# Kernel optimization log

Hardware: AMD Instinct MI355X
Metric: run time of the kernel (lower is better)

The kernel has to match this reference:

```python
import jax, jax.numpy as jnp
import numpy as np

NOISE_EPS = 1e-2   # Shazeer noisy-gating stddev floor
LN_EPS = 1e-6
LOSS_COEF = 0.01
K = 2              # num_activated_experts


def _layer_norm(x, w, b):
    mu = jnp.mean(x, axis=-1, keepdims=True)
    var = jnp.var(x, axis=-1, keepdims=True)
    return (x - mu) * jax.lax.rsqrt(var + LN_EPS) * w + b


def _cv_squared(v):
    return jnp.var(v) / (jnp.mean(v) ** 2 + 1e-10)


def _normal_cdf(z):
    return 0.5 * (1.0 + jax.scipy.special.erf(z / jnp.sqrt(jnp.asarray(2.0, z.dtype))))


def setup_inputs() -> dict:
    key = jax.random.key(0)
    ks = jax.random.split(key, 8)
    N, D, H, O, E = 8192, 512, 1024, 512, 8
    x = jax.random.normal(ks[0], (N, D), jnp.float32)
    x_offsets = jnp.sort(jax.random.randint(ks[1], (17,), 0, N)).astype(jnp.int64)
    noise = jax.random.normal(ks[2], (N, E), jnp.float32)
    s = 0.02
    return {
        "x": x,
        "x_offsets": x_offsets,
        "max_seq_len": 2048,
        "noise": noise,
        "norm_w": jnp.ones((D,), jnp.float32),
        "norm_bias": jnp.zeros((D,), jnp.float32),
        "w_gate": jax.random.normal(ks[3], (D, E), jnp.float32) * s,
        "w_noise": jax.random.normal(ks[4], (D, E), jnp.float32) * s,
        "W1": jax.random.normal(ks[5], (E, H, D), jnp.float32) * s,  # [E, model_d, input]
        "b1": jnp.zeros((E, H), jnp.float32),
        "W2": jax.random.normal(ks[6], (E, O, H), jnp.float32) * s,  # [E, output, model_d]
        "b2": jnp.zeros((E, O), jnp.float32),
        "output_weight": jax.random.normal(ks[7], (D, O), jnp.float32) * s,
    }


def reference(x, x_offsets, max_seq_len, noise, norm_w, norm_bias, w_gate, w_noise,
              W1, b1, W2, b2, output_weight):
    N, D = x.shape
    E = w_gate.shape[1]
    k_plus = min(K + 1, E)

    # pre-norm
    x_norm = _layer_norm(x, norm_w, norm_bias)

    # noisy top-k gating (training path)
    clean_logits = x_norm @ w_gate                      # [N, E]
    noise_stddev = jax.nn.softplus(x_norm @ w_noise) + NOISE_EPS
    noisy_logits = clean_logits + noise * noise_stddev

    top_logits, top_indices = jax.lax.top_k(noisy_logits, k_plus)   # [N, k+1]
    top_k_logits = top_logits[:, :K]
    top_k_indices = top_indices[:, :K]
    top_k_gates = jax.nn.softmax(top_k_logits, axis=-1)             # [N, K]

    rows = jnp.arange(N)[:, None]
    gates = jnp.zeros((N, E), top_k_gates.dtype).at[rows, top_k_indices].set(top_k_gates)

    # load = prob each expert is in top-k under the gating noise (Shazeer)
    flat = top_logits.reshape(-1)
    pos_in = jnp.arange(N) * k_plus + K
    thr_in = flat[pos_in][:, None]          # (k+1)-th value: threshold if already in
    thr_out = flat[pos_in - 1][:, None]     # k-th value: threshold if currently out
    is_in = noisy_logits > thr_in
    prob_in = _normal_cdf((clean_logits - thr_in) / noise_stddev)
    prob_out = _normal_cdf((clean_logits - thr_out) / noise_stddev)
    load_probs = jnp.where(is_in, prob_in, prob_out)                # [N, E]

    loss = LOSS_COEF * (_cv_squared(gates.sum(0)) + _cv_squared(load_probs.sum(0)))

    # dispatch stats: tokens per expert
    lengths = jnp.zeros((E,), jnp.float32).at[top_k_indices.reshape(-1)].add(1.0)
    load = lengths / lengths.sum()

    # grouped expert MLP (dense one-hot combine; gates are 0 for unrouted experts)
    h = jnp.einsum('nd,ehd->neh', x_norm, W1) + b1                  # [N, E, H]
    a = jax.nn.silu(h)
    y_e = jnp.einsum('neh,eoh->neo', a, W2) + b2                    # [N, E, O]
    y_moe = jnp.einsum('ne,neo->no', gates, y_e)                    # [N, O]

    # shared expert: addmm(y, shared_x=x, output_weight)
    y = y_moe + x @ output_weight
    return y, loss, load
```

## Files before the change

kernel.cpp:

```cpp
#include <hip/hip_runtime.h>
#include <math.h>

typedef unsigned short u16;
typedef unsigned int u32;

#define N_ROWS 8192
#define DDIM 512
#define HDIM 1024
#define ODIM 512
#define NEXP 8
#define MAXPAIRS (N_ROWS * 2)
#define MAXPOS (MAXPAIRS + NEXP * 128)
#define MAXTILES (MAXPOS / 128)

#define SM_CNT 0
#define SM_CUR 8
#define SM_AOFF 16
#define SM_GSUM 32
#define SM_LSUM 40
#define SM_WORDS 64

using short8 = __attribute__((ext_vector_type(8))) short;
using float4v = __attribute__((ext_vector_type(4))) float;

__device__ __forceinline__ u16 f2bf(float f) {
    union { float f; u32 u; } v; v.f = f;
    u32 u = v.u;
    return (u16)((u + 0x7fffu + ((u >> 16) & 1u)) >> 16);
}

__device__ __forceinline__ void async_copy16(u16* lds, const u16* g) {
    __builtin_amdgcn_global_load_lds(
        (const __attribute__((address_space(1))) void*)g,
        (__attribute__((address_space(3))) void*)lds, 16, 0, 0);
}

__global__ __launch_bounds__(512) void init1_kernel(int* small, float* zeropage) {
    int i = threadIdx.x;
    if (i < SM_WORDS) small[i] = 0;
    zeropage[i] = 0.f;
}

#define W1CONV_BLOCKS 4096
#define GATE_BLOCKS 512
#define OWT_BLOCKS 256
#define BUCKET_BLOCKS 68
#define YZERO_BLOCKS 1024
__global__ __launch_bounds__(256) void combo_kernel(
    const float* __restrict__ x, const float* __restrict__ noise,
    const float* __restrict__ norm_w, const float* __restrict__ norm_b,
    const float* __restrict__ w_gate, const float* __restrict__ w_noise,
    const float* __restrict__ W1, const float* __restrict__ ow,
    u16* __restrict__ xnorm_bf, u16* __restrict__ x_bf,
    int* __restrict__ pair_expert, float* __restrict__ pair_gate,
    u16* __restrict__ W1b, u16* __restrict__ owT,
    int* __restrict__ small, int* __restrict__ bucket_rows, float* __restrict__ y)
{
    __shared__ __align__(16) float sh[NEXP * DDIM * 2 + 64];
    int b = blockIdx.x, tid = threadIdx.x;

    if (b >= GATE_BLOCKS) {
        int cb = b - GATE_BLOCKS;
        if (cb < W1CONV_BLOCKS) {
            size_t i = (size_t)cb * 256 + tid;
            float4 v = ((const float4*)W1)[i];
            ushort4 o;
            o.x = f2bf(v.x); o.y = f2bf(v.y); o.z = f2bf(v.z); o.w = f2bf(v.w);
            ((ushort4*)W1b)[i] = o;
        } else if (cb < W1CONV_BLOCKS + OWT_BLOCKS) {
            float (*tile)[33] = (float(*)[33])sh;
            int t = cb - W1CONV_BLOCKS;
            int bx = (t & 15) * 32, by = (t >> 4) * 32;
            int tx = tid & 31, ty = tid >> 5;
            for (int r = ty; r < 32; r += 8) tile[r][tx] = ow[(size_t)(by + r) * ODIM + bx + tx];
            __syncthreads();
            for (int r = ty; r < 32; r += 8) owT[(size_t)(bx + r) * DDIM + by + tx] = f2bf(tile[tx][r]);
        } else if (cb < W1CONV_BLOCKS + OWT_BLOCKS + BUCKET_BLOCKS) {
            int i = (cb - W1CONV_BLOCKS - OWT_BLOCKS) * 256 + tid;
            if (i < MAXPOS) bucket_rows[i] = -1;
        } else {
            int zb = cb - W1CONV_BLOCKS - OWT_BLOCKS - BUCKET_BLOCKS;
            size_t i = (size_t)zb * 1024 + tid;
            float4 zero = {0.f, 0.f, 0.f, 0.f};
#pragma unroll
            for (int t = 0; t < 4; t++, i += 256) ((float4*)y)[i] = zero;
        }
        return;
    }

    float* wgT = sh;
    float* wnT = sh + NEXP * DDIM;
    float* blk_g = sh + 2 * NEXP * DDIM;
    float* blk_l = blk_g + NEXP;
    int* blk_c = (int*)(blk_l + NEXP);
    float* smf = (float*)small;

    for (int i = tid; i < NEXP * DDIM; i += 256) {
        int d = i >> 3, e = i & 7;
        wgT[e * DDIM + d] = w_gate[i];
        wnT[e * DDIM + d] = w_noise[i];
    }
    if (tid < NEXP) { blk_g[tid] = 0.f; blk_l[tid] = 0.f; blk_c[tid] = 0; }
    __syncthreads();

    int wave = tid >> 6, lane = tid & 63;
    float nw[8], nb[8];
#pragma unroll
    for (int j = 0; j < 8; j++) { nw[j] = norm_w[j * 64 + lane]; nb[j] = norm_b[j * 64 + lane]; }

    for (int r = 0; r < 4; ++r) {
        int row = b * 16 + wave * 4 + r;
        const float* xr = x + (size_t)row * DDIM;
        float xv[8], s = 0.f, s2 = 0.f;
#pragma unroll
        for (int j = 0; j < 8; j++) { float v = xr[j * 64 + lane]; xv[j] = v; s += v; s2 += v * v; }
#pragma unroll
        for (int o = 32; o; o >>= 1) { s += __shfl_xor(s, o, 64); s2 += __shfl_xor(s2, o, 64); }
        float mu = s * (1.f / DDIM);
        float var = s2 * (1.f / DDIM) - mu * mu;
        float rstd = rsqrtf(var + 1e-6f);

        float acc[16];
#pragma unroll
        for (int e = 0; e < 16; e++) acc[e] = 0.f;
#pragma unroll
        for (int j = 0; j < 8; j++) {
            float v = (xv[j] - mu) * rstd * nw[j] + nb[j];
            int d = j * 64 + lane;
            xnorm_bf[(size_t)row * DDIM + d] = f2bf(v);
            x_bf[(size_t)row * DDIM + d] = f2bf(xv[j]);
#pragma unroll
            for (int e = 0; e < 8; e++) {
                acc[e] += v * wgT[e * DDIM + d];
                acc[8 + e] += v * wnT[e * DDIM + d];
            }
        }
#pragma unroll
        for (int e = 0; e < 16; e++)
#pragma unroll
            for (int o = 32; o; o >>= 1) acc[e] += __shfl_xor(acc[e], o, 64);

        float cl[8], sd[8], nz[8];
#pragma unroll
        for (int e = 0; e < 8; e++) {
            cl[e] = acc[e];
            float t = acc[8 + e];
            float sp = fmaxf(t, 0.f) + log1pf(expf(-fabsf(t)));
            sd[e] = sp + 0.01f;
            nz[e] = cl[e] + noise[(size_t)row * NEXP + e] * sd[e];
        }
        int idx[3]; float val[3]; u32 msk = 0;
#pragma unroll
        for (int t = 0; t < 3; t++) {
            float best = -INFINITY; int bi = 0;
#pragma unroll
            for (int e = 0; e < 8; e++)
                if (!((msk >> e) & 1) && nz[e] > best) { best = nz[e]; bi = e; }
            idx[t] = bi; val[t] = best; msk |= 1u << bi;
        }
        float e1 = expf(val[1] - val[0]);
        float g0 = 1.f / (1.f + e1), g1 = e1 / (1.f + e1);
        float thr_in = val[2], thr_out = val[1];

        if (lane == 0) {
            pair_expert[row * 2] = idx[0]; pair_gate[row * 2] = g0;
            pair_expert[row * 2 + 1] = idx[1]; pair_gate[row * 2 + 1] = g1;
            atomicAdd(&blk_g[idx[0]], g0); atomicAdd(&blk_g[idx[1]], g1);
            atomicAdd(&blk_c[idx[0]], 1); atomicAdd(&blk_c[idx[1]], 1);
#pragma unroll
            for (int e = 0; e < 8; e++) {
                float thr = (nz[e] > thr_in) ? thr_in : thr_out;
                float z = (cl[e] - thr) / sd[e];
                float p = 0.5f * (1.f + erff(z * 0.70710678118654752f));
                atomicAdd(&blk_l[e], p);
            }
        }
    }
    __syncthreads();
    if (tid < NEXP) {
        atomicAdd(smf + SM_GSUM + tid, blk_g[tid]);
        atomicAdd(smf + SM_LSUM + tid, blk_l[tid]);
        atomicAdd(&small[SM_CNT + tid], blk_c[tid]);
    }
}

__global__ __launch_bounds__(256) void scatter_kernel(
    const int* __restrict__ pair_expert, const float* __restrict__ pair_gate,
    int* __restrict__ small, int* __restrict__ bucket_rows, float* __restrict__ gate_by_pos,
    float* __restrict__ out_loss, float* __restrict__ out_load)
{
    __shared__ int aoff[NEXP + 1];
    __shared__ int blk_cnt[NEXP];
    __shared__ int blk_base[NEXP];
    int tid = threadIdx.x;
    if (tid == 0) {
        int acc = 0; aoff[0] = 0;
        for (int e = 0; e < NEXP; e++) { acc += (small[SM_CNT + e] + 127) & ~127; aoff[e + 1] = acc; }
    }
    if (tid < NEXP) blk_cnt[tid] = 0;
    __syncthreads();
    int p = blockIdx.x * 256 + tid;
    int e = pair_expert[p];
    int local = atomicAdd(&blk_cnt[e], 1);
    __syncthreads();
    if (tid < NEXP)
        blk_base[tid] = aoff[tid] + atomicAdd(&small[SM_CUR + tid], blk_cnt[tid]);
    if (blockIdx.x == 0 && tid < NEXP + 1) small[SM_AOFF + tid] = aoff[tid];
    __syncthreads();
    int pos = blk_base[e] + local;
    bucket_rows[pos] = p >> 1;
    gate_by_pos[pos] = pair_gate[p];

    if (blockIdx.x == 0 && tid == 0) {
        const float* gs = (const float*)small + SM_GSUM;
        const float* ls = (const float*)small + SM_LSUM;
        float cv[2];
        for (int t = 0; t < 2; t++) {
            const float* v = t ? ls : gs;
            float m = 0.f;
            for (int k = 0; k < NEXP; k++) m += v[k];
            m *= (1.f / NEXP);
            float var = 0.f;
            for (int k = 0; k < NEXP; k++) { float d = v[k] - m; var += d * d; }
            var *= (1.f / NEXP);
            cv[t] = var / (m * m + 1e-10f);
        }
        out_loss[0] = 0.01f * (cv[0] + cv[1]);
        int tot = 0;
        for (int k = 0; k < NEXP; k++) tot += small[SM_CNT + k];
        float inv = 1.f / (float)tot;
        for (int k = 0; k < NEXP; k++) out_load[k] = (float)small[SM_CNT + k] * inv;
    }
}

__global__ __launch_bounds__(256) void gemmA_kernel(
    const u16* __restrict__ xnorm, const u16* __restrict__ W1b,
    const float* __restrict__ W2, u16* __restrict__ W2b,
    const int* __restrict__ bucket_rows, const int* __restrict__ small,
    const float* __restrict__ b1, const u16* __restrict__ zeropage,
    u16* __restrict__ a_buf)
{
    constexpr int KD = 512;
    __shared__ __align__(16) u16 As[128 * 64];
    __shared__ __align__(16) u16 Bs[128 * 64];

    int tid = threadIdx.x;
    if (blockIdx.y >= 8) {
        int j = (blockIdx.y - 8) * 136 + blockIdx.x;
        if (j >= 2048) return;
        size_t i = (size_t)j * 512 + tid;
#pragma unroll
        for (int t = 0; t < 2; t++, i += 256) {
            float4 v = ((const float4*)W2)[i];
            ushort4 o;
            o.x = f2bf(v.x); o.y = f2bf(v.y); o.z = f2bf(v.z); o.w = f2bf(v.w);
            ((ushort4*)W2b)[i] = o;
        }
        return;
    }

    int base = blockIdx.x * 128;
    if (base >= small[SM_AOFF + 8]) return;
    int e = 0;
    while (e < 7 && base >= small[SM_AOFF + e + 1]) ++e;
    int bn = blockIdx.y * 128;
    const u16* Bsel = W1b + (size_t)e * HDIM * KD;

    int wave = tid >> 6, lane = tid & 63;
    int lr = lane >> 3;
    int lc = ((lane & 7) ^ lr) * 8;

    const u16* ga[4]; const u16* gb[4];
    u16* la[4]; u16* lb[4];
#pragma unroll
    for (int c = 0; c < 4; c++) {
        int tr = wave * 32 + c * 8;
        int r0 = bucket_rows[base + tr + lr];
        ga[c] = ((r0 < 0) ? zeropage : xnorm + (size_t)r0 * KD) + lc;
        gb[c] = Bsel + (size_t)(bn + tr + lr) * KD + lc;
        la[c] = &As[tr * 64];
        lb[c] = &Bs[tr * 64];
    }

    int wm = (wave & 1) * 64, wn = (wave >> 1) * 64;
    int fr = lane & 15, kq = lane >> 4, f7 = fr & 7;

    float4v acc[4][4];
#pragma unroll
    for (int i = 0; i < 4; i++)
#pragma unroll
        for (int j = 0; j < 4; j++) acc[i][j] = (float4v){0.f, 0.f, 0.f, 0.f};

    for (int k0 = 0; k0 < KD; k0 += 64) {
        __syncthreads();
#pragma unroll
        for (int c = 0; c < 4; c++) async_copy16(la[c], ga[c] + k0);
#pragma unroll
        for (int c = 0; c < 4; c++) async_copy16(lb[c], gb[c] + k0);
        __syncthreads();
        short8 af[4][2], bf[4][2];
#pragma unroll
        for (int mt = 0; mt < 4; mt++)
#pragma unroll
            for (int kh = 0; kh < 2; kh++)
                af[mt][kh] = *(const short8*)&As[(wm + mt * 16 + fr) * 64 + (((kq + 4 * kh) ^ f7) * 8)];
#pragma unroll
        for (int nt = 0; nt < 4; nt++)
#pragma unroll
            for (int kh = 0; kh < 2; kh++)
                bf[nt][kh] = *(const short8*)&Bs[(wn + nt * 16 + fr) * 64 + (((kq + 4 * kh) ^ f7) * 8)];
#pragma unroll
        for (int mt = 0; mt < 4; mt++)
#pragma unroll
            for (int nt = 0; nt < 4; nt++) {
                acc[mt][nt] = __builtin_amdgcn_mfma_f32_16x16x32_bf16(af[mt][0], bf[nt][0], acc[mt][nt], 0, 0, 0);
                acc[mt][nt] = __builtin_amdgcn_mfma_f32_16x16x32_bf16(af[mt][1], bf[nt][1], acc[mt][nt], 0, 0, 0);
            }
    }

    int rbase = (lane >> 4) * 4, c16 = lane & 15;
#pragma unroll
    for (int nt = 0; nt < 4; nt++) {
        int gn = bn + wn + nt * 16 + c16;
        float bv = b1[e * HDIM + gn];
#pragma unroll
        for (int mt = 0; mt < 4; mt++) {
            int gm = base + wm + mt * 16 + rbase;
#pragma unroll
            for (int r = 0; r < 4; r++) {
                float h = acc[mt][nt][r] + bv;
                float a = h * __builtin_amdgcn_rcpf(1.f + __expf(-h));
                a_buf[(size_t)(gm + r) * HDIM + gn] = f2bf(a);
            }
        }
    }
}

__global__ __launch_bounds__(256) void gemmB_kernel(
    const u16* __restrict__ a_buf, const u16* __restrict__ W2b,
    const u16* __restrict__ xbf, const u16* __restrict__ owT,
    const int* __restrict__ bucket_rows, const int* __restrict__ small,
    const float* __restrict__ b2, const float* __restrict__ gate_by_pos,
    float* __restrict__ y)
{
    __shared__ __align__(16) u16 As[2][128 * 32];
    __shared__ __align__(16) u16 Bs[2][128 * 32];

    int tid = threadIdx.x;
    int wave = tid >> 6, lane = tid & 63;
    const int lrow = lane >> 2;
    const int kcol = (((lane & 3) ^ ((lane >> 3) & 3)) * 8);
    const int trow = wave * 32 + lrow;
    int wm = (wave & 1) * 64, wn = (wave >> 1) * 64;
    int fr = lane & 15, kq = lane >> 4;
    const int kg = ((kq ^ ((fr >> 1) & 3)) * 8);

    bool expertPath = blockIdx.y < 4;
    int base, bn, e = 0, KD;
    const u16 *ga0, *ga1, *gb0, *gb1;
    if (expertPath) {
        KD = 1024;
        base = blockIdx.x * 128;
        if (base >= small[SM_AOFF + 8]) return;
        while (e < 7 && base >= small[SM_AOFF + e + 1]) ++e;
        bn = blockIdx.y * 128;
        ga0 = a_buf + (size_t)(base + trow) * KD + kcol;
        ga1 = a_buf + (size_t)(base + trow + 16) * KD + kcol;
        const u16* Bsel = W2b + (size_t)e * ODIM * KD;
        gb0 = Bsel + (size_t)(bn + trow) * KD + kcol;
        gb1 = Bsel + (size_t)(bn + trow + 16) * KD + kcol;
    } else {
        KD = 512;
        int j = (blockIdx.y - 4) * 136 + blockIdx.x;
        if (j >= 256) return;
        base = (j >> 2) * 128;
        bn = (j & 3) * 128;
        ga0 = xbf + (size_t)(base + trow) * KD + kcol;
        ga1 = xbf + (size_t)(base + trow + 16) * KD + kcol;
        gb0 = owT + (size_t)(bn + trow) * KD + kcol;
        gb1 = owT + (size_t)(bn + trow + 16) * KD + kcol;
    }
    const int ofA0 = (wave * 32) * 32;
    const int ofA1 = (wave * 32 + 16) * 32;

    float4v acc[4][4];
#pragma unroll
    for (int i = 0; i < 4; i++)
#pragma unroll
        for (int j = 0; j < 4; j++) acc[i][j] = (float4v){0.f, 0.f, 0.f, 0.f};

    const int nk = KD >> 5;
    async_copy16(&As[0][ofA0], ga0);
    async_copy16(&As[0][ofA1], ga1);
    async_copy16(&Bs[0][ofA0], gb0);
    async_copy16(&Bs[0][ofA1], gb1);
    __syncthreads();

    int cur = 0;
    for (int t = 0; t < nk; ++t) {
        int nxt = cur ^ 1;
        if (t + 1 < nk) {
            int k1 = (t + 1) << 5;
            async_copy16(&As[nxt][ofA0], ga0 + k1);
            async_copy16(&As[nxt][ofA1], ga1 + k1);
            async_copy16(&Bs[nxt][ofA0], gb0 + k1);
            async_copy16(&Bs[nxt][ofA1], gb1 + k1);
        }
        short8 af[4], bf[4];
#pragma unroll
        for (int mt = 0; mt < 4; mt++) af[mt] = *(const short8*)&As[cur][(wm + mt * 16 + fr) * 32 + kg];
#pragma unroll
        for (int nt = 0; nt < 4; nt++) bf[nt] = *(const short8*)&Bs[cur][(wn + nt * 16 + fr) * 32 + kg];
#pragma unroll
        for (int mt = 0; mt < 4; mt++)
#pragma unroll
            for (int nt = 0; nt < 4; nt++)
                acc[mt][nt] = __builtin_amdgcn_mfma_f32_16x16x32_bf16(af[mt], bf[nt], acc[mt][nt], 0, 0, 0);
        __syncthreads();
        cur = nxt;
    }

    int rbase = (lane >> 4) * 4, c16 = lane & 15;
    if (expertPath) {
#pragma unroll
        for (int mt = 0; mt < 4; mt++) {
            int pos0 = base + wm + mt * 16 + rbase;
            int rows[4]; float gs[4];
#pragma unroll
            for (int r = 0; r < 4; r++) { rows[r] = bucket_rows[pos0 + r]; gs[r] = gate_by_pos[pos0 + r]; }
#pragma unroll
            for (int nt = 0; nt < 4; nt++) {
                int gn = bn + wn + nt * 16 + c16;
                float b2v = b2[e * ODIM + gn];
#pragma unroll
                for (int r = 0; r < 4; r++) {
                    if (rows[r] >= 0)
                        unsafeAtomicAdd(&y[(size_t)rows[r] * ODIM + gn], gs[r] * (acc[mt][nt][r] + b2v));
                }
            }
        }
    } else {
#pragma unroll
        for (int mt = 0; mt < 4; mt++) {
            int gm = base + wm + mt * 16 + rbase;
#pragma unroll
            for (int nt = 0; nt < 4; nt++) {
                int gn = bn + wn + nt * 16 + c16;
#pragma unroll
                for (int r = 0; r < 4; r++)
                    unsafeAtomicAdd(&y[(size_t)(gm + r) * ODIM + gn], acc[mt][nt][r]);
            }
        }
    }
}

extern "C" void kernel_launch(void* const* d_in, const int* in_sizes, int n_in,
                              void* d_out, int out_size, void* d_ws, size_t ws_size,
                              hipStream_t stream)
{
    (void)in_sizes; (void)n_in; (void)out_size; (void)ws_size;
    const float* x = (const float*)d_in[0];
    const float* noise = (const float*)d_in[3];
    const float* norm_w = (const float*)d_in[4];
    const float* norm_b = (const float*)d_in[5];
    const float* w_gate = (const float*)d_in[6];
    const float* w_noise = (const float*)d_in[7];
    const float* W1 = (const float*)d_in[8];
    const float* b1 = (const float*)d_in[9];
    const float* W2 = (const float*)d_in[10];
    const float* b2 = (const float*)d_in[11];
    const float* ow = (const float*)d_in[12];

    float* y = (float*)d_out;
    float* out_loss = y + (size_t)N_ROWS * ODIM;
    float* out_load = out_loss + 1;

    char* ws = (char*)d_ws;
    size_t off = 0;
    auto alloc = [&](size_t b) { size_t p = off; off = (off + b + 255) & ~(size_t)255; return p; };
    u16* xnorm_bf = (u16*)(ws + alloc((size_t)N_ROWS * DDIM * 2));
    u16* x_bf     = (u16*)(ws + alloc((size_t)N_ROWS * DDIM * 2));
    u16* W1b      = (u16*)(ws + alloc((size_t)NEXP * HDIM * DDIM * 2));
    u16* W2b      = (u16*)(ws + alloc((size_t)NEXP * ODIM * HDIM * 2));
    u16* owT      = (u16*)(ws + alloc((size_t)DDIM * ODIM * 2));
    u16* a_buf    = (u16*)(ws + alloc((size_t)MAXPOS * HDIM * 2));
    int* pair_expert = (int*)(ws + alloc((size_t)MAXPAIRS * 4));
    float* pair_gate = (float*)(ws + alloc((size_t)MAXPAIRS * 4));
    float* gate_by_pos = (float*)(ws + alloc((size_t)MAXPOS * 4));
    int* bucket_rows = (int*)(ws + alloc((size_t)MAXPOS * 4));
    int* small       = (int*)(ws + alloc(SM_WORDS * 4));
    float* zeropage  = (float*)(ws + alloc(2048));

    init1_kernel<<<1, 512, 0, stream>>>(small, zeropage);
    combo_kernel<<<GATE_BLOCKS + W1CONV_BLOCKS + OWT_BLOCKS + BUCKET_BLOCKS + YZERO_BLOCKS,
                   256, 0, stream>>>(
        x, noise, norm_w, norm_b, w_gate, w_noise, W1, ow,
        xnorm_bf, x_bf, pair_expert, pair_gate, W1b, owT, small, bucket_rows, y);
    scatter_kernel<<<MAXPAIRS / 256, 256, 0, stream>>>(pair_expert, pair_gate, small,
                                                       bucket_rows, gate_by_pos, out_loss, out_load);
    gemmA_kernel<<<dim3(MAXTILES, 8 + 16), 256, 0, stream>>>(xnorm_bf, W1b, W2, W2b,
                                                             bucket_rows, small, b1,
                                                             (const u16*)zeropage, a_buf);
    gemmB_kernel<<<dim3(MAXTILES, 6), 256, 0, stream>>>(a_buf, W2b, x_bf, owT, bucket_rows,
                                                        small, b2, gate_by_pos, y);
}
```

Before: 247.1 us.

## Triple-buffer LDS tiles in both expert GEMMs with a single-barrier prefetch pipeline

Both grouped GEMM kernels move to a three-stage shared-memory ring of 32-wide K slices. Loads are issued two slices ahead, and each iteration waits with a partial vmcnt and a single barrier. The first GEMM was previously unpipelined, with two syncthreads and no overlap. The change also raises wave priority around the MFMA block with s_setprio. The goal is to hide global-to-LDS latency behind the matrix math, at the cost of more shared memory per block and reliance on hand-placed waitcnt counts being correct.

Result: slower. 281.5 us (+13.9%).

```diff
diff --git a/kernel.cpp b/kernel.cpp
--- a/kernel.cpp
+++ b/kernel.cpp
@@ -241,8 +241,8 @@
     u16* __restrict__ a_buf)
 {
     constexpr int KD = 512;
-    __shared__ __align__(16) u16 As[128 * 64];
-    __shared__ __align__(16) u16 Bs[128 * 64];
+    __shared__ __align__(16) u16 As[3][128 * 32];
+    __shared__ __align__(16) u16 Bs[3][128 * 32];
 
     int tid = threadIdx.x;
     if (blockIdx.y >= 8) {
@@ -267,23 +267,21 @@
     const u16* Bsel = W1b + (size_t)e * HDIM * KD;
 
     int wave = tid >> 6, lane = tid & 63;
-    int lr = lane >> 3;
-    int lc = ((lane & 7) ^ lr) * 8;
-
-    const u16* ga[4]; const u16* gb[4];
-    u16* la[4]; u16* lb[4];
-#pragma unroll
-    for (int c = 0; c < 4; c++) {
-        int tr = wave * 32 + c * 8;
-        int r0 = bucket_rows[base + tr + lr];
-        ga[c] = ((r0 < 0) ? zeropage : xnorm + (size_t)r0 * KD) + lc;
-        gb[c] = Bsel + (size_t)(bn + tr + lr) * KD + lc;
-        la[c] = &As[tr * 64];
-        lb[c] = &Bs[tr * 64];
-    }
-
+    const int lrow = lane >> 2;
+    const int kcol = (((lane & 3) ^ ((lane >> 3) & 3)) * 8);
+    const int trow = wave * 32 + lrow;
     int wm = (wave & 1) * 64, wn = (wave >> 1) * 64;
-    int fr = lane & 15, kq = lane >> 4, f7 = fr & 7;
+    int fr = lane & 15, kq = lane >> 4;
+    const int kg = ((kq ^ ((fr >> 1) & 3)) * 8);
+
+    int r0 = bucket_rows[base + trow];
+    int r1 = bucket_rows[base + trow + 16];
+    const u16* ga0 = ((r0 < 0) ? zeropage : xnorm + (size_t)r0 * KD) + kcol;
+    const u16* ga1 = ((r1 < 0) ? zeropage : xnorm + (size_t)r1 * KD) + kcol;
+    const u16* gb0 = Bsel + (size_t)(bn + trow) * KD + kcol;
+    const u16* gb1 = Bsel + (size_t)(bn + trow + 16) * KD + kcol;
+    const int ofA0 = (wave * 32) * 32;
+    const int ofA1 = (wave * 32 + 16) * 32;
 
     float4v acc[4][4];
 #pragma unroll
@@ -291,31 +289,37 @@
 #pragma unroll
         for (int j = 0; j < 4; j++) acc[i][j] = (float4v){0.f, 0.f, 0.f, 0.f};
 
-    for (int k0 = 0; k0 < KD; k0 += 64) {
-        __syncthreads();
-#pragma unroll
-        for (int c = 0; c < 4; c++) async_copy16(la[c], ga[c] + k0);
-#pragma unroll
-        for (int c = 0; c < 4; c++) async_copy16(lb[c], gb[c] + k0);
-        __syncthreads();
-        short8 af[4][2], bf[4][2];
+    constexpr int nk = KD >> 5;
+    async_copy16(&As[0][ofA0], ga0);      async_copy16(&As[0][ofA1], ga1);
+    async_copy16(&Bs[0][ofA0], gb0);      async_copy16(&Bs[0][ofA1], gb1);
+    async_copy16(&As[1][ofA0], ga0 + 32); async_copy16(&As[1][ofA1], ga1 + 32);
+    async_copy16(&Bs[1][ofA0], gb0 + 32); async_copy16(&Bs[1][ofA1], gb1 + 32);
+
+    int cur = 0;
+    for (int t = 0; t < nk; ++t) {
+        if (t == nk - 1) asm volatile("s_waitcnt vmcnt(0)" ::: "memory");
+        else             asm volatile("s_waitcnt vmcnt(4)" ::: "memory");
+        __builtin_amdgcn_s_barrier();
+        __builtin_amdgcn_sched_barrier(0);
+        if (t + 2 < nk) {
+            int b = cur + 2; if (b >= 3) b -= 3;
+            int k2 = (t + 2) << 5;
+            async_copy16(&As[b][ofA0], ga0 + k2); async_copy16(&As[b][ofA1], ga1 + k2);
+            async_copy16(&Bs[b][ofA0], gb0 + k2); async_copy16(&Bs[b][ofA1], gb1 + k2);
+        }
+        short8 af[4], bf[4];
+#pragma unroll
+        for (int mt = 0; mt < 4; mt++) af[mt] = *(const short8*)&As[cur][(wm + mt * 16 + fr) * 32 + kg];
+#pragma unroll
+        for (int nt = 0; nt < 4; nt++) bf[nt] = *(const short8*)&Bs[cur][(wn + nt * 16 + fr) * 32 + kg];
+        __builtin_amdgcn_s_setprio(1);
 #pragma unroll
         for (int mt = 0; mt < 4; mt++)
 #pragma unroll
-            for (int kh = 0; kh < 2; kh++)
-                af[mt][kh] = *(const short8*)&As[(wm + mt * 16 + fr) * 64 + (((kq + 4 * kh) ^ f7) * 8)];
-#pragma unroll
-        for (int nt = 0; nt < 4; nt++)
-#pragma unroll
-            for (int kh = 0; kh < 2; kh++)
-                bf[nt][kh] = *(const short8*)&Bs[(wn + nt * 16 + fr) * 64 + (((kq + 4 * kh) ^ f7) * 8)];
-#pragma unroll
-        for (int mt = 0; mt < 4; mt++)
-#pragma unroll
-            for (int nt = 0; nt < 4; nt++) {
-                acc[mt][nt] = __builtin_amdgcn_mfma_f32_16x16x32_bf16(af[mt][0], bf[nt][0], acc[mt][nt], 0, 0, 0);
-                acc[mt][nt] = __builtin_amdgcn_mfma_f32_16x16x32_bf16(af[mt][1], bf[nt][1], acc[mt][nt], 0, 0, 0);
-            }
+            for (int nt = 0; nt < 4; nt++)
+                acc[mt][nt] = __builtin_amdgcn_mfma_f32_16x16x32_bf16(af[mt], bf[nt], acc[mt][nt], 0, 0, 0);
+        __builtin_amdgcn_s_setprio(0);
+        cur = cur + 1; if (cur >= 3) cur = 0;
     }
 
     int rbase = (lane >> 4) * 4, c16 = lane & 15;
@@ -343,8 +347,8 @@
     const float* __restrict__ b2, const float* __restrict__ gate_by_pos,
     float* __restrict__ y)
 {
-    __shared__ __align__(16) u16 As[2][128 * 32];
-    __shared__ __align__(16) u16 Bs[2][128 * 32];
+    __shared__ __align__(16) u16 As[3][128 * 32];
+    __shared__ __align__(16) u16 Bs[3][128 * 32];
 
     int tid = threadIdx.x;
     int wave = tid >> 6, lane = tid & 63;
@@ -390,34 +394,36 @@
         for (int j = 0; j < 4; j++) acc[i][j] = (float4v){0.f, 0.f, 0.f, 0.f};
 
     const int nk = KD >> 5;
-    async_copy16(&As[0][ofA0], ga0);
-    async_copy16(&As[0][ofA1], ga1);
-    async_copy16(&Bs[0][ofA0], gb0);
-    async_copy16(&Bs[0][ofA1], gb1);
-    __syncthreads();
+    async_copy16(&As[0][ofA0], ga0);      async_copy16(&As[0][ofA1], ga1);
+    async_copy16(&Bs[0][ofA0], gb0);      async_copy16(&Bs[0][ofA1], gb1);
+    async_copy16(&As[1][ofA0], ga0 + 32); async_copy16(&As[1][ofA1], ga1 + 32);
+    async_copy16(&Bs[1][ofA0], gb0 + 32); async_copy16(&Bs[1][ofA1], gb1 + 32);
 
     int cur = 0;
     for (int t = 0; t < nk; ++t) {
-        int nxt = cur ^ 1;
-        if (t + 1 < nk) {
-            int k1 = (t + 1) << 5;
-            async_copy16(&As[nxt][ofA0], ga0 + k1);
-            async_copy16(&As[nxt][ofA1], ga1 + k1);
-            async_copy16(&Bs[nxt][ofA0], gb0 + k1);
-            async_copy16(&Bs[nxt][ofA1], gb1 + k1);
+        if (t == nk - 1) asm volatile("s_waitcnt vmcnt(0)" ::: "memory");
+        else             asm volatile("s_waitcnt vmcnt(4)" ::: "memory");
+        __builtin_amdgcn_s_barrier();
+        __builtin_amdgcn_sched_barrier(0);
+        if (t + 2 < nk) {
+            int b = cur + 2; if (b >= 3) b -= 3;
+            int k2 = (t + 2) << 5;
+            async_copy16(&As[b][ofA0], ga0 + k2); async_copy16(&As[b][ofA1], ga1 + k2);
+            async_copy16(&Bs[b][ofA0], gb0 + k2); async_copy16(&Bs[b][ofA1], gb1 + k2);
         }
         short8 af[4], bf[4];
 #pragma unroll
         for (int mt = 0; mt < 4; mt++) af[mt] = *(const short8*)&As[cur][(wm + mt * 16 + fr) * 32 + kg];
 #pragma unroll
         for (int nt = 0; nt < 4; nt++) bf[nt] = *(const short8*)&Bs[cur][(wn + nt * 16 + fr) * 32 + kg];
+        __builtin_amdgcn_s_setprio(1);
 #pragma unroll
         for (int mt = 0; mt < 4; mt++)
 #pragma unroll
             for (int nt = 0; nt < 4; nt++)
                 acc[mt][nt] = __builtin_amdgcn_mfma_f32_16x16x32_bf16(af[mt], bf[nt], acc[mt][nt], 0, 0, 0);
-        __syncthreads();
-        cur = nxt;
+        __builtin_amdgcn_s_setprio(0);
+        cur = cur + 1; if (cur >= 3) cur = 0;
     }
 
     int rbase = (lane >> 4) * 4, c16 = lane & 15;
```

## Move shared-expert GEMM into gemmA with plain stores; shrink gemmB tiles to 64 rows

Applied to the files above, without the earlier changes.

The shared-expert x@output_weight GEMM moves from gemmB into extra blocks of gemmA. It now writes y with plain stores, which replaces both the separate y-zeroing blocks in combo_kernel and the atomic adds for that term. gemmB now handles only the expert path, using 64-row M tiles and twice as many M blocks, to improve load balance and occupancy over the ragged per-expert buckets. This depends on gemmA's plain stores to y being ordered before gemmB's atomics by stream order. The smaller tiles also lower data reuse per block.

Measured after the change: 252.0 us. 1.02x slower.

```diff
diff --git a/kernel.cpp b/kernel.cpp
--- a/kernel.cpp
+++ b/kernel.cpp
@@ -12,6 +12,7 @@
 #define MAXPAIRS (N_ROWS * 2)
 #define MAXPOS (MAXPAIRS + NEXP * 128)
 #define MAXTILES (MAXPOS / 128)
+#define MAXTILES64 (MAXPOS / 64)
 
 #define SM_CNT 0
 #define SM_CUR 8
@@ -45,7 +46,6 @@
 #define GATE_BLOCKS 512
 #define OWT_BLOCKS 256
 #define BUCKET_BLOCKS 68
-#define YZERO_BLOCKS 1024
 __global__ __launch_bounds__(256) void combo_kernel(
     const float* __restrict__ x, const float* __restrict__ noise,
     const float* __restrict__ norm_w, const float* __restrict__ norm_b,
@@ -54,7 +54,7 @@
     u16* __restrict__ xnorm_bf, u16* __restrict__ x_bf,
     int* __restrict__ pair_expert, float* __restrict__ pair_gate,
     u16* __restrict__ W1b, u16* __restrict__ owT,
-    int* __restrict__ small, int* __restrict__ bucket_rows, float* __restrict__ y)
+    int* __restrict__ small, int* __restrict__ bucket_rows)
 {
     __shared__ __align__(16) float sh[NEXP * DDIM * 2 + 64];
     int b = blockIdx.x, tid = threadIdx.x;
@@ -75,15 +75,9 @@
             for (int r = ty; r < 32; r += 8) tile[r][tx] = ow[(size_t)(by + r) * ODIM + bx + tx];
             __syncthreads();
             for (int r = ty; r < 32; r += 8) owT[(size_t)(bx + r) * DDIM + by + tx] = f2bf(tile[tx][r]);
-        } else if (cb < W1CONV_BLOCKS + OWT_BLOCKS + BUCKET_BLOCKS) {
+        } else {
             int i = (cb - W1CONV_BLOCKS - OWT_BLOCKS) * 256 + tid;
             if (i < MAXPOS) bucket_rows[i] = -1;
-        } else {
-            int zb = cb - W1CONV_BLOCKS - OWT_BLOCKS - BUCKET_BLOCKS;
-            size_t i = (size_t)zb * 1024 + tid;
-            float4 zero = {0.f, 0.f, 0.f, 0.f};
-#pragma unroll
-            for (int t = 0; t < 4; t++, i += 256) ((float4*)y)[i] = zero;
         }
         return;
     }
@@ -236,15 +230,81 @@
 __global__ __launch_bounds__(256) void gemmA_kernel(
     const u16* __restrict__ xnorm, const u16* __restrict__ W1b,
     const float* __restrict__ W2, u16* __restrict__ W2b,
+    const u16* __restrict__ xbf, const u16* __restrict__ owT,
     const int* __restrict__ bucket_rows, const int* __restrict__ small,
     const float* __restrict__ b1, const u16* __restrict__ zeropage,
-    u16* __restrict__ a_buf)
+    u16* __restrict__ a_buf, float* __restrict__ y)
 {
     constexpr int KD = 512;
     __shared__ __align__(16) u16 As[128 * 64];
     __shared__ __align__(16) u16 Bs[128 * 64];
 
     int tid = threadIdx.x;
+    if (blockIdx.y >= 24) {
+        int j = (blockIdx.y - 24) * 136 + blockIdx.x;
+        if (j >= 256) return;
+        int base = (j >> 2) * 128, bn = (j & 3) * 128;
+        int wave = tid >> 6, lane = tid & 63;
+        const int lrow = lane >> 2;
+        const int kcol = (((lane & 3) ^ ((lane >> 3) & 3)) * 8);
+        const int trow = wave * 32 + lrow;
+        int wm = (wave & 1) * 64, wn = (wave >> 1) * 64;
+        int fr = lane & 15, kq = lane >> 4;
+        const int kg = ((kq ^ ((fr >> 1) & 3)) * 8);
+        const u16* ga0 = xbf + (size_t)(base + trow) * KD + kcol;
+        const u16* ga1 = xbf + (size_t)(base + trow + 16) * KD + kcol;
+        const u16* gb0 = owT + (size_t)(bn + trow) * KD + kcol;
+        const u16* gb1 = owT + (size_t)(bn + trow + 16) * KD + kcol;
+        u16* As2 = (u16*)As; u16* Bs2 = (u16*)Bs;
+        const int ofA0 = (wave * 32) * 32, ofA1 = (wave * 32 + 16) * 32;
+
+        float4v acc[4][4];
+#pragma unroll
+        for (int i = 0; i < 4; i++)
+#pragma unroll
+            for (int jj = 0; jj < 4; jj++) acc[i][jj] = (float4v){0.f, 0.f, 0.f, 0.f};
+
+        async_copy16(As2 + ofA0, ga0); async_copy16(As2 + ofA1, ga1);
+        async_copy16(Bs2 + ofA0, gb0); async_copy16(Bs2 + ofA1, gb1);
+        __syncthreads();
+        int cur = 0;
+        for (int t = 0; t < 16; ++t) {
+            int nxt = cur ^ 1;
+            if (t + 1 < 16) {
+                int k1 = (t + 1) << 5;
+                async_copy16(As2 + nxt * 4096 + ofA0, ga0 + k1);
+                async_copy16(As2 + nxt * 4096 + ofA1, ga1 + k1);
+                async_copy16(Bs2 + nxt * 4096 + ofA0, gb0 + k1);
+                async_copy16(Bs2 + nxt * 4096 + ofA1, gb1 + k1);
+            }
+            short8 af[4], bf[4];
+#pragma unroll
+            for (int mt = 0; mt < 4; mt++) af[mt] = *(const short8*)&As2[cur * 4096 + (wm + mt * 16 + fr) * 32 + kg];
+#pragma unroll
+            for (int nt = 0; nt < 4; nt++) bf[nt] = *(const short8*)&Bs2[cur * 4096 + (wn + nt * 16 + fr) * 32 + kg];
+#pragma unroll
+            for (int mt = 0; mt < 4; mt++)
+#pragma unroll
+                for (int nt = 0; nt < 4; nt++)
+                    acc[mt][nt] = __builtin_amdgcn_mfma_f32_16x16x32_bf16(af[mt], bf[nt], acc[mt][nt], 0, 0, 0);
+            __syncthreads();
+            cur = nxt;
+        }
+        int rbase = (lane >> 4) * 4, c16 = lane & 15;
+#pragma unroll
+        for (int mt = 0; mt < 4; mt++) {
+            int gm = base + wm + mt * 16 + rbase;
+#pragma unroll
+            for (int nt = 0; nt < 4; nt++) {
+                int gn = bn + wn + nt * 16 + c16;
+#pragma unroll
+                for (int r = 0; r < 4; r++)
+                    y[(size_t)(gm + r) * ODIM + gn] = acc[mt][nt][r];
+            }
+        }
+        return;
+    }
+
     if (blockIdx.y >= 8) {
         int j = (blockIdx.y - 8) * 136 + blockIdx.x;
         if (j >= 2048) return;
@@ -338,62 +398,46 @@
 
 __global__ __launch_bounds__(256) void gemmB_kernel(
     const u16* __restrict__ a_buf, const u16* __restrict__ W2b,
-    const u16* __restrict__ xbf, const u16* __restrict__ owT,
     const int* __restrict__ bucket_rows, const int* __restrict__ small,
     const float* __restrict__ b2, const float* __restrict__ gate_by_pos,
     float* __restrict__ y)
 {
-    __shared__ __align__(16) u16 As[2][128 * 32];
+    constexpr int KD = 1024;
+    __shared__ __align__(16) u16 As[2][64 * 32];
     __shared__ __align__(16) u16 Bs[2][128 * 32];
 
     int tid = threadIdx.x;
     int wave = tid >> 6, lane = tid & 63;
     const int lrow = lane >> 2;
     const int kcol = (((lane & 3) ^ ((lane >> 3) & 3)) * 8);
-    const int trow = wave * 32 + lrow;
-    int wm = (wave & 1) * 64, wn = (wave >> 1) * 64;
+    int wm = (wave >> 1) * 32, wn = (wave & 1) * 64;
     int fr = lane & 15, kq = lane >> 4;
     const int kg = ((kq ^ ((fr >> 1) & 3)) * 8);
 
-    bool expertPath = blockIdx.y < 4;
-    int base, bn, e = 0, KD;
-    const u16 *ga0, *ga1, *gb0, *gb1;
-    if (expertPath) {
-        KD = 1024;
-        base = blockIdx.x * 128;
-        if (base >= small[SM_AOFF + 8]) return;
-        while (e < 7 && base >= small[SM_AOFF + e + 1]) ++e;
-        bn = blockIdx.y * 128;
-        ga0 = a_buf + (size_t)(base + trow) * KD + kcol;
-        ga1 = a_buf + (size_t)(base + trow + 16) * KD + kcol;
-        const u16* Bsel = W2b + (size_t)e * ODIM * KD;
-        gb0 = Bsel + (size_t)(bn + trow) * KD + kcol;
-        gb1 = Bsel + (size_t)(bn + trow + 16) * KD + kcol;
-    } else {
-        KD = 512;
-        int j = (blockIdx.y - 4) * 136 + blockIdx.x;
-        if (j >= 256) return;
-        base = (j >> 2) * 128;
-        bn = (j & 3) * 128;
-        ga0 = xbf + (size_t)(base + trow) * KD + kcol;
-        ga1 = xbf + (size_t)(base + trow + 16) * KD + kcol;
-        gb0 = owT + (size_t)(bn + trow) * KD + kcol;
-        gb1 = owT + (size_t)(bn + trow + 16) * KD + kcol;
-    }
-    const int ofA0 = (wave * 32) * 32;
-    const int ofA1 = (wave * 32 + 16) * 32;
-
-    float4v acc[4][4];
-#pragma unroll
-    for (int i = 0; i < 4; i++)
+    int base = blockIdx.x * 64;
+    if (base >= small[SM_AOFF + 8]) return;
+    int e = 0;
+    while (e < 7 && base >= small[SM_AOFF + e + 1]) ++e;
+    int bn = blockIdx.y * 128;
+
+    const u16* ga0 = a_buf + (size_t)(base + wave * 16 + lrow) * KD + kcol;
+    const u16* Bsel = W2b + (size_t)e * ODIM * KD;
+    const u16* gb0 = Bsel + (size_t)(bn + wave * 32 + lrow) * KD + kcol;
+    const u16* gb1 = Bsel + (size_t)(bn + wave * 32 + 16 + lrow) * KD + kcol;
+    const int ofA = (wave * 16) * 32;
+    const int ofB0 = (wave * 32) * 32;
+    const int ofB1 = (wave * 32 + 16) * 32;
+
+    float4v acc[2][4];
+#pragma unroll
+    for (int i = 0; i < 2; i++)
 #pragma unroll
         for (int j = 0; j < 4; j++) acc[i][j] = (float4v){0.f, 0.f, 0.f, 0.f};
 
-    const int nk = KD >> 5;
-    async_copy16(&As[0][ofA0], ga0);
-    async_copy16(&As[0][ofA1], ga1);
-    async_copy16(&Bs[0][ofA0], gb0);
-    async_copy16(&Bs[0][ofA1], gb1);
+    constexpr int nk = KD >> 5;
+    async_copy16(&As[0][ofA], ga0);
+    async_copy16(&Bs[0][ofB0], gb0);
+    async_copy16(&Bs[0][ofB1], gb1);
     __syncthreads();
 
     int cur = 0;
@@ -401,18 +445,17 @@
         int nxt = cur ^ 1;
         if (t + 1 < nk) {
             int k1 = (t + 1) << 5;
-            async_copy16(&As[nxt][ofA0], ga0 + k1);
-            async_copy16(&As[nxt][ofA1], ga1 + k1);
-            async_copy16(&Bs[nxt][ofA0], gb0 + k1);
-            async_copy16(&Bs[nxt][ofA1], gb1 + k1);
-        }
-        short8 af[4], bf[4];
-#pragma unroll
-        for (int mt = 0; mt < 4; mt++) af[mt] = *(const short8*)&As[cur][(wm + mt * 16 + fr) * 32 + kg];
+            async_copy16(&As[nxt][ofA], ga0 + k1);
+            async_copy16(&Bs[nxt][ofB0], gb0 + k1);
+            async_copy16(&Bs[nxt][ofB1], gb1 + k1);
+        }
+        short8 af[2], bf[4];
+#pragma unroll
+        for (int mt = 0; mt < 2; mt++) af[mt] = *(const short8*)&As[cur][(wm + mt * 16 + fr) * 32 + kg];
 #pragma unroll
         for (int nt = 0; nt < 4; nt++) bf[nt] = *(const short8*)&Bs[cur][(wn + nt * 16 + fr) * 32 + kg];
 #pragma unroll
-        for (int mt = 0; mt < 4; mt++)
+        for (int mt = 0; mt < 2; mt++)
 #pragma unroll
             for (int nt = 0; nt < 4; nt++)
                 acc[mt][nt] = __builtin_amdgcn_mfma_f32_16x16x32_bf16(af[mt], bf[nt], acc[mt][nt], 0, 0, 0);
@@ -421,34 +464,20 @@
     }
 
     int rbase = (lane >> 4) * 4, c16 = lane & 15;
-    if (expertPath) {
-#pragma unroll
-        for (int mt = 0; mt < 4; mt++) {
-            int pos0 = base + wm + mt * 16 + rbase;
-            int rows[4]; float gs[4];
-#pragma unroll
-            for (int r = 0; r < 4; r++) { rows[r] = bucket_rows[pos0 + r]; gs[r] = gate_by_pos[pos0 + r]; }
-#pragma unroll
-            for (int nt = 0; nt < 4; nt++) {
-                int gn = bn + wn + nt * 16 + c16;
-                float b2v = b2[e * ODIM + gn];
-#pragma unroll
-                for (int r = 0; r < 4; r++) {
-                    if (rows[r] >= 0)
-                        unsafeAtomicAdd(&y[(size_t)rows[r] * ODIM + gn], gs[r] * (acc[mt][nt][r] + b2v));
-                }
-            }
-        }
-    } else {
-#pragma unroll
-        for (int mt = 0; mt < 4; mt++) {
-            int gm = base + wm + mt * 16 + rbase;
-#pragma unroll
-            for (int nt = 0; nt < 4; nt++) {
-                int gn = bn + wn + nt * 16 + c16;
-#pragma unroll
-                for (int r = 0; r < 4; r++)
-                    unsafeAtomicAdd(&y[(size_t)(gm + r) * ODIM + gn], acc[mt][nt][r]);
+#pragma unroll
+    for (int mt = 0; mt < 2; mt++) {
+        int pos0 = base + wm + mt * 16 + rbase;
+        int rows[4]; float gs[4];
+#pragma unroll
+        for (int r = 0; r < 4; r++) { rows[r] = bucket_rows[pos0 + r]; gs[r] = gate_by_pos[pos0 + r]; }
+#pragma unroll
+        for (int nt = 0; nt < 4; nt++) {
+            int gn = bn + wn + nt * 16 + c16;
+            float b2v = b2[e * ODIM + gn];
+#pragma unroll
+            for (int r = 0; r < 4; r++) {
+                if (rows[r] >= 0)
+                    unsafeAtomicAdd(&y[(size_t)rows[r] * ODIM + gn], gs[r] * (acc[mt][nt][r] + b2v));
             }
         }
     }
@@ -492,15 +521,15 @@
     float* zeropage  = (float*)(ws + alloc(2048));
 
     init1_kernel<<<1, 512, 0, stream>>>(small, zeropage);
-    combo_kernel<<<GATE_BLOCKS + W1CONV_BLOCKS + OWT_BLOCKS + BUCKET_BLOCKS + YZERO_BLOCKS,
+    combo_kernel<<<GATE_BLOCKS + W1CONV_BLOCKS + OWT_BLOCKS + BUCKET_BLOCKS,
                    256, 0, stream>>>(
         x, noise, norm_w, norm_b, w_gate, w_noise, W1, ow,
-        xnorm_bf, x_bf, pair_expert, pair_gate, W1b, owT, small, bucket_rows, y);
+        xnorm_bf, x_bf, pair_expert, pair_gate, W1b, owT, small, bucket_rows);
     scatter_kernel<<<MAXPAIRS / 256, 256, 0, stream>>>(pair_expert, pair_gate, small,
                                                        bucket_rows, gate_by_pos, out_loss, out_load);
-    gemmA_kernel<<<dim3(MAXTILES, 8 + 16), 256, 0, stream>>>(xnorm_bf, W1b, W2, W2b,
-                                                             bucket_rows, small, b1,
-                                                             (const u16*)zeropage, a_buf);
-    gemmB_kernel<<<dim3(MAXTILES, 6), 256, 0, stream>>>(a_buf, W2b, x_bf, owT, bucket_rows,
-                                                        small, b2, gate_by_pos, y);
-}
+    gemmA_kernel<<<dim3(MAXTILES, 8 + 16 + 2), 256, 0, stream>>>(xnorm_bf, W1b, W2, W2b,
+                                                                 x_bf, owT, bucket_rows, small, b1,
+                                                                 (const u16*)zeropage, a_buf, y);
+    gemmB_kernel<<<dim3(MAXTILES64, 4), 256, 0, stream>>>(a_buf, W2b, bucket_rows,
+                                                          small, b2, gate_by_pos, y);
+}
```
